# Performance work log

Hardware: AMD Instinct MI355X
Metric: run time of the kernel (lower is better)

The kernel has to match this reference:

```python
import jax, jax.numpy as jnp
import numpy as np

TAU = 0.5
LOGIT_TAU = float(np.log(TAU / (1.0 - TAU)))  # = 0.0 for tau=0.5
N_STEPS = 128           # torch samples randint(128,129) -> always 128
N_SECANT = 8
D_MIN, D_MAX = 0.0, 2.4
B, N, HID, CDIM = 4, 8192, 64, 128


def decoder(p, c, W1, Wc, b1, W2, b2):
    """Occupancy-logit MLP. p: (B, ..., 3), c: (B, CDIM) -> (B, ...)."""
    cc = c @ Wc  # (B, HID)
    cc = cc.reshape(cc.shape[:1] + (1,) * (p.ndim - 2) + cc.shape[1:])
    h = jax.nn.relu(jnp.einsum('...d,dh->...h', p, W1) + cc + b1)
    return (h @ W2 + b2)[..., 0]


def setup_inputs() -> dict:
    key = jax.random.key(0)
    ks = jax.random.split(key, 8)
    return {
        'ray0': jax.random.normal(ks[0], (B, N, 3), jnp.float32) * 0.5,
        'ray_direction': jax.random.normal(ks[1], (B, N, 3), jnp.float32),
        'c': jax.random.normal(ks[2], (B, CDIM), jnp.float32),
        'W1': jax.random.normal(ks[3], (3, HID), jnp.float32) * 0.5,
        'Wc': jax.random.normal(ks[4], (CDIM, HID), jnp.float32) * 0.1,
        'b1': jax.random.normal(ks[5], (HID,), jnp.float32) * 0.1,
        'W2': jax.random.normal(ks[6], (HID, 1), jnp.float32) * 0.5,
        'b2': jax.random.normal(ks[7], (1,), jnp.float32) * 0.1,
    }


def reference(ray0, ray_direction, c, W1, Wc, b1, W2, b2):
    S = N_STEPS
    bsz, npts, _ = ray0.shape
    dec = lambda p: decoder(p, c, W1, Wc, b1, W2, b2)

    # --- coarse ray marching ---
    d_prop = jnp.linspace(D_MIN, D_MAX, S).astype(ray0.dtype)        # (S,)
    p_prop = ray0[:, :, None, :] + ray_direction[:, :, None, :] * d_prop[None, None, :, None]
    val = dec(p_prop) - LOGIT_TAU                                    # (B, N, S)

    mask_0_not_occupied = val[:, :, 0] < 0
    sign_matrix = jnp.concatenate(
        [jnp.sign(val[:, :, :-1] * val[:, :, 1:]),
         jnp.ones((bsz, npts, 1), val.dtype)], axis=-1)
    cost_matrix = sign_matrix * jnp.arange(S, 0, -1, dtype=val.dtype)
    indices = jnp.argmin(cost_matrix, axis=-1)                       # (B, N)
    values = jnp.min(cost_matrix, axis=-1)
    mask_sign_change = values < 0
    f_low = jnp.take_along_axis(val, indices[..., None], axis=2)[..., 0]
    mask_neg_to_pos = f_low < 0
    mask = mask_sign_change & mask_neg_to_pos & mask_0_not_occupied

    d_prop_full = jnp.broadcast_to(d_prop, (bsz, npts, S))
    d_low = jnp.take_along_axis(d_prop_full, indices[..., None], axis=2)[..., 0]
    idx_hi = jnp.minimum(indices + 1, S - 1)
    d_high = jnp.take_along_axis(d_prop_full, idx_hi[..., None], axis=2)[..., 0]
    f_high = jnp.take_along_axis(val, idx_hi[..., None], axis=2)[..., 0]

    # safe placeholders for non-surface rays (results discarded by mask)
    d_low = jnp.where(mask, d_low, 0.0)
    d_high = jnp.where(mask, d_high, 1.0)
    f_low = jnp.where(mask, f_low, -1.0)
    f_high = jnp.where(mask, f_high, 1.0)

    # --- secant refinement (vectorized over all rays) ---
    d_pred = -f_low * (d_high - d_low) / (f_high - f_low) + d_low
    for _ in range(N_SECANT):
        p_mid = ray0 + d_pred[..., None] * ray_direction
        f_mid = dec(p_mid) - LOGIT_TAU
        ind_low = f_mid < 0
        d_low = jnp.where(ind_low, d_pred, d_low)
        f_low = jnp.where(ind_low, f_mid, f_low)
        d_high = jnp.where(ind_low, d_high, d_pred)
        f_high = jnp.where(ind_low, f_high, f_mid)
        d_pred = -f_low * (d_high - d_low) / (f_high - f_low) + d_low

    d_out = jnp.where(mask, d_pred, jnp.inf)
    d_out = jnp.where(mask_0_not_occupied, d_out, 0.0)
    return d_out
```

## Files before the change

### kernel.cpp

```cpp
#include <hip/hip_runtime.h>
#include <hip/hip_bf16.h>

#define HID   64
#define CDIM  128
#define NSTEP 128
#define NRAYS 32768

#define STEPF (2.4f / 127.0f)

typedef const __hip_bfloat16* __restrict__ bf16p;

__device__ __forceinline__ float bf2f(__hip_bfloat16 x) { return __bfloat162float(x); }

__global__ __launch_bounds__(256) void depth_fused(
    bf16p ray0, bf16p rdir, bf16p c, bf16p W1, bf16p Wc, bf16p b1, bf16p W2,
    bf16p b2, __hip_bfloat16* __restrict__ out) {
    __shared__ __align__(16) float4 sAB[4][4][HID];
    __shared__ float4 sW4[4][HID];
    __shared__ float  sCB[4][HID];
    __shared__ float  part[4][HID];

    const int tid   = threadIdx.x;
    const int wave  = tid >> 6;
    const int lane  = tid & 63;
    const int rbase = blockIdx.x * 16 + wave * 4;
    const int batch = blockIdx.x >> 9;

    const float b2v = bf2f(b2[0]);

    const float wx  = bf2f(W1[lane]);
    const float wy  = bf2f(W1[HID + lane]);
    const float wz  = bf2f(W1[2 * HID + lane]);
    const float w2l = bf2f(W2[lane]);
    sW4[wave][lane] = make_float4(wx, wy, wz, w2l);

    {
        float acc = 0.0f;
        const __hip_bfloat16* crow = c + batch * CDIM;
        const int k0 = wave * 32;
#pragma unroll
        for (int k = 0; k < 32; ++k)
            acc = fmaf(bf2f(crow[k0 + k]), bf2f(Wc[(k0 + k) * HID + lane]), acc);
        part[wave][lane] = acc;
    }
    __syncthreads();
    const float cbv = bf2f(b1[lane]) +
        ((part[0][lane] + part[1][lane]) + (part[2][lane] + part[3][lane]));
    sCB[wave][lane] = cbv;

    {
#pragma unroll
        for (int t = 0; t < 4; ++t) {
            const int r = rbase + t;
            const float ox = bf2f(ray0[r * 3 + 0]), oy = bf2f(ray0[r * 3 + 1]), oz = bf2f(ray0[r * 3 + 2]);
            const float dx = bf2f(rdir[r * 3 + 0]), dy = bf2f(rdir[r * 3 + 1]), dz = bf2f(rdir[r * 3 + 2]);
            const float a  = fmaf(ox, wx, fmaf(oy, wy, fmaf(oz, wz, cbv)));
            const float bb = fmaf(dx, wx, fmaf(dy, wy, dz * wz));
            sAB[wave][t][lane] = make_float4(a, bb, w2l, 0.0f);
        }
    }

    const int t = lane >> 4;
    const int g = lane & 15;

    float d[8], v[8];
#pragma unroll
    for (int k = 0; k < 8; ++k) {
        d[k] = bf2f(__float2bfloat16((float)(8 * g + k) * STEPF));
        v[k] = b2v;
    }

    const float4* __restrict__ row = &sAB[wave][t][0];
#pragma unroll
    for (int j = 0; j < HID; ++j) {
        const float4 abw = row[j];
#pragma unroll
        for (int k = 0; k < 8; ++k) {
            float h = fmaf(d[k], abw.y, abw.x);
            v[k] = fmaf(fmaxf(h, 0.0f), abw.z, v[k]);
        }
    }

    float nv = __shfl_down(v[0], 1);
    float key;
#pragma unroll
    for (int k = 0; k < 8; ++k) {
        const int s = 8 * g + k;
        float vn = (k < 7) ? v[k + 1] : nv;
        float prod = v[k] * vn;
        float sgn = (prod < 0.0f) ? -1.0f : ((prod > 0.0f) ? 1.0f : 0.0f);
        float kk = (s == NSTEP - 1) ? (256.0f + 127.0f)
                                    : fmaf(sgn * (float)(NSTEP - s), 256.0f, (float)s);
        key = (k == 0) ? kk : fminf(key, kk);
    }
#pragma unroll
    for (int off = 1; off < 16; off <<= 1)
        key = fminf(key, __shfl_xor(key, off));
    const float cf = floorf(key * 0.00390625f);
    const int   mi = (int)(key - cf * 256.0f);

    const int idx  = mi;
    const int idxh = (idx + 1 < NSTEP) ? idx + 1 : NSTEP - 1;
    const int q  = idx  & 7, qh = idxh & 7;

    float cand = v[0], candh = v[0];
#pragma unroll
    for (int k = 1; k < 8; ++k) {
        cand  = (q  == k) ? v[k] : cand;
        candh = (qh == k) ? v[k] : candh;
    }
    const int lane_lo = (lane & 48) | (idx  >> 3);
    const int lane_hi = (lane & 48) | (idxh >> 3);
    float f_low  = __shfl(cand,  lane_lo);
    float f_high = __shfl(candh, lane_hi);
    float v00    = __shfl(v[0], lane & 48);

    bool m0   = v00 < 0.0f;
    bool mask = (key < 0.0f) && (f_low < 0.0f) && m0;

    if (!mask && g == 0) {
        out[rbase + t] = __float2bfloat16(m0 ? 0x1.FEp127f : 0.0f);
    }

    if (__ballot(mask)) {
        const int r = rbase + t;
        const float ox = bf2f(ray0[r * 3 + 0]), oy = bf2f(ray0[r * 3 + 1]), oz = bf2f(ray0[r * 3 + 2]);
        const float dx = bf2f(rdir[r * 3 + 0]), dy = bf2f(rdir[r * 3 + 1]), dz = bf2f(rdir[r * 3 + 2]);

        float dl = bf2f(__float2bfloat16(idx  * STEPF));
        float dh = bf2f(__float2bfloat16(idxh * STEPF));
        float fl = f_low, fh = f_high;

        float4 Wm[4];
        float  cbm[4];
#pragma unroll
        for (int m = 0; m < 4; ++m) {
            Wm[m]  = sW4[wave][g + 16 * m];
            cbm[m] = sCB[wave][g + 16 * m];
        }

        float dp = -fl * (dh - dl) / (fh - fl) + dl;
#pragma unroll
        for (int it = 0; it < 8; ++it) {
            const float px = fmaf(dp, dx, ox), py = fmaf(dp, dy, oy), pz = fmaf(dp, dz, oz);
            float s = 0.0f;
#pragma unroll
            for (int m = 0; m < 4; ++m) {
                float h = fmaf(px, Wm[m].x, fmaf(py, Wm[m].y, fmaf(pz, Wm[m].z, cbm[m])));
                s = fmaf(fmaxf(h, 0.0f), Wm[m].w, s);
            }
#pragma unroll
            for (int off = 1; off < 16; off <<= 1)
                s += __shfl_xor(s, off);
            const float fm = s + b2v;
            const bool lowside = fm < 0.0f;
            dl = lowside ? dp : dl;
            fl = lowside ? fm : fl;
            dh = lowside ? dh : dp;
            fh = lowside ? fh : fm;
            dp = -fl * (dh - dl) / (fh - fl) + dl;
        }
        if (mask && g == 0) out[r] = __float2bfloat16(dp);
    }
}

extern "C" void kernel_launch(void* const* d_in, const int* in_sizes, int n_in,
                              void* d_out, int out_size, void* d_ws, size_t ws_size,
                              hipStream_t stream) {
    bf16p ray0 = (bf16p)d_in[0];
    bf16p rdir = (bf16p)d_in[1];
    bf16p c    = (bf16p)d_in[2];
    bf16p W1   = (bf16p)d_in[3];
    bf16p Wc   = (bf16p)d_in[4];
    bf16p b1   = (bf16p)d_in[5];
    bf16p W2   = (bf16p)d_in[6];
    bf16p b2   = (bf16p)d_in[7];
    __hip_bfloat16* out = (__hip_bfloat16*)d_out;
    (void)d_ws; (void)ws_size;

    hipLaunchKernelGGL(depth_fused, dim3(NRAYS / 16), dim3(256), 0, stream,
                       ray0, rdir, c, W1, Wc, b1, W2, b2, out);
}
```

Baseline: 89.14 us.

## Evaluate coarse march MLP in packed fp16 with v_pk_max relu

Replaces the fp32 coarse ray-march MLP loop with packed half2 math. Pairs of hidden units are processed per instruction using hfma2 and a v_pk_max_f16 relu, with A/B/W2 terms stored as fp16 in shared memory and loaded 16 bytes at a time. The aim is to roughly halve the ALU work in the dominant 128-step evaluation. In exchange, fp16 accumulation over 64 hidden units may flip sign-change detection near zero crossings, and shared W/cb arrays are now written redundantly by all waves without a race-free guarantee, though the values written are identical.

```diff
diff --git a/kernel.cpp b/kernel.cpp
--- a/kernel.cpp
+++ b/kernel.cpp
@@ -1,5 +1,6 @@
 #include <hip/hip_runtime.h>
 #include <hip/hip_bf16.h>
+#include <hip/hip_fp16.h>
 
 #define HID   64
 #define CDIM  128
@@ -12,12 +13,20 @@
 
 __device__ __forceinline__ float bf2f(__hip_bfloat16 x) { return __bfloat162float(x); }
 
+__device__ __forceinline__ __half2 pk_relu(__half2 h) {
+    unsigned hu = __builtin_bit_cast(unsigned, h);
+    asm("v_pk_max_f16 %0, %1, %2" : "=v"(hu) : "v"(hu), "v"(0u));
+    return __builtin_bit_cast(__half2, hu);
+}
+
 __global__ __launch_bounds__(256) void depth_fused(
     bf16p ray0, bf16p rdir, bf16p c, bf16p W1, bf16p Wc, bf16p b1, bf16p W2,
     bf16p b2, __hip_bfloat16* __restrict__ out) {
-    __shared__ __align__(16) float4 sAB[4][4][HID];
-    __shared__ float4 sW4[4][HID];
-    __shared__ float  sCB[4][HID];
+    __shared__ __align__(16) unsigned short sA16[4][4][80];
+    __shared__ __align__(16) unsigned short sB16[4][4][80];
+    __shared__ __align__(16) unsigned short sW2h[64];
+    __shared__ float4 sW4sh[HID];
+    __shared__ float  sCBsh[HID];
     __shared__ float  part[4][HID];
 
     const int tid   = threadIdx.x;
@@ -32,7 +41,8 @@
     const float wy  = bf2f(W1[HID + lane]);
     const float wz  = bf2f(W1[2 * HID + lane]);
     const float w2l = bf2f(W2[lane]);
-    sW4[wave][lane] = make_float4(wx, wy, wz, w2l);
+    sW4sh[lane] = make_float4(wx, wy, wz, w2l);
+    sW2h[lane]  = __half_as_ushort(__float2half(w2l));
 
     {
         float acc = 0.0f;
@@ -46,7 +56,7 @@
     __syncthreads();
     const float cbv = bf2f(b1[lane]) +
         ((part[0][lane] + part[1][lane]) + (part[2][lane] + part[3][lane]));
-    sCB[wave][lane] = cbv;
+    sCBsh[lane] = cbv;
 
     {
 #pragma unroll
@@ -56,30 +66,51 @@
             const float dx = bf2f(rdir[r * 3 + 0]), dy = bf2f(rdir[r * 3 + 1]), dz = bf2f(rdir[r * 3 + 2]);
             const float a  = fmaf(ox, wx, fmaf(oy, wy, fmaf(oz, wz, cbv)));
             const float bb = fmaf(dx, wx, fmaf(dy, wy, dz * wz));
-            sAB[wave][t][lane] = make_float4(a, bb, w2l, 0.0f);
+            sA16[wave][t][lane] = __half_as_ushort(__float2half(a));
+            sB16[wave][t][lane] = __half_as_ushort(__float2half(bb));
         }
     }
 
     const int t = lane >> 4;
     const int g = lane & 15;
 
-    float d[8], v[8];
+    __half2 d2[8], acc2[8];
+    const __half2 zero2 = __float2half2_rn(0.0f);
 #pragma unroll
     for (int k = 0; k < 8; ++k) {
-        d[k] = bf2f(__float2bfloat16((float)(8 * g + k) * STEPF));
-        v[k] = b2v;
-    }
-
-    const float4* __restrict__ row = &sAB[wave][t][0];
-#pragma unroll
-    for (int j = 0; j < HID; ++j) {
-        const float4 abw = row[j];
-#pragma unroll
-        for (int k = 0; k < 8; ++k) {
-            float h = fmaf(d[k], abw.y, abw.x);
-            v[k] = fmaf(fmaxf(h, 0.0f), abw.z, v[k]);
-        }
-    }
+        d2[k]   = __float2half2_rn(bf2f(__float2bfloat16((float)(8 * g + k) * STEPF)));
+        acc2[k] = zero2;
+    }
+
+    const unsigned short* __restrict__ rowA = &sA16[wave][t][0];
+    const unsigned short* __restrict__ rowB = &sB16[wave][t][0];
+    const unsigned short* __restrict__ rowW = &sW2h[0];
+#pragma unroll
+    for (int blk = 0; blk < 8; ++blk) {
+        const float4 a4 = *(const float4*)(rowA + 8 * blk);
+        const float4 b4 = *(const float4*)(rowB + 8 * blk);
+        const float4 w4 = *(const float4*)(rowW + 8 * blk);
+        const float av[4] = {a4.x, a4.y, a4.z, a4.w};
+        const float bv[4] = {b4.x, b4.y, b4.z, b4.w};
+        const float wv[4] = {w4.x, w4.y, w4.z, w4.w};
+#pragma unroll
+        for (int p = 0; p < 4; ++p) {
+            const __half2 ap = __builtin_bit_cast(__half2, av[p]);
+            const __half2 bp = __builtin_bit_cast(__half2, bv[p]);
+            const __half2 wp = __builtin_bit_cast(__half2, wv[p]);
+#pragma unroll
+            for (int k = 0; k < 8; ++k) {
+                __half2 h = __hfma2(d2[k], bp, ap);
+                h = pk_relu(h);
+                acc2[k] = __hfma2(h, wp, acc2[k]);
+            }
+        }
+    }
+
+    float v[8];
+#pragma unroll
+    for (int k = 0; k < 8; ++k)
+        v[k] = b2v + __low2float(acc2[k]) + __high2float(acc2[k]);
 
     float nv = __shfl_down(v[0], 1);
     float key;
@@ -135,8 +166,8 @@
         float  cbm[4];
 #pragma unroll
         for (int m = 0; m < 4; ++m) {
-            Wm[m]  = sW4[wave][g + 16 * m];
-            cbm[m] = sCB[wave][g + 16 * m];
+            Wm[m]  = sW4sh[g + 16 * m];
+            cbm[m] = sCBsh[g + 16 * m];
         }
 
         float dp = -fl * (dh - dl) / (fh - fl) + dl;
```

After: 83.68 us. 1.07x faster.
